# Performance work log

Hardware: AMD Instinct MI355X
Metric: run time of the kernel (lower is better)

## Reference

```python
import jax, jax.numpy as jnp
import numpy as np

N = 100000      # nodes
E = 1600000     # edges (avg degree 16)
IN = 128        # in_channels
OUT = 32        # out_channels -> hidden = 2*OUT = 64


def gcn_conv(x, src, dst, W, b):
    """PyG GCNConv: linear transform, add self loops, symmetric D^-1/2 (A+I) D^-1/2 aggregation."""
    n = x.shape[0]
    h = x @ W                                   # [N, out]
    # degree with self loops (all edge weights = 1)
    deg = jax.ops.segment_sum(jnp.ones(src.shape[0], h.dtype), dst, num_segments=n) + 1.0
    dinv = jax.lax.rsqrt(deg)                   # [N]
    norm = dinv[src] * dinv[dst]                # [E]
    agg = jax.ops.segment_sum(h[src] * norm[:, None], dst, num_segments=n)
    agg = agg + h * (dinv * dinv)[:, None]      # self-loop contribution
    return agg + b


def setup_inputs() -> dict:
    key = jax.random.key(0)
    ks = jax.random.split(key, 8)
    x = jax.random.normal(ks[0], (N, IN), jnp.float32)
    edge_index = jax.random.randint(ks[1], (2, E), 0, N, jnp.int32)
    H = 2 * OUT
    W1 = jax.random.normal(ks[2], (IN, H), jnp.float32) / jnp.sqrt(jnp.float32(IN))
    b1 = jnp.zeros((H,), jnp.float32)
    W_mu = jax.random.normal(ks[3], (H, OUT), jnp.float32) / jnp.sqrt(jnp.float32(H))
    b_mu = jnp.zeros((OUT,), jnp.float32)
    W_logstd = jax.random.normal(ks[4], (H, OUT), jnp.float32) / jnp.sqrt(jnp.float32(H))
    b_logstd = jnp.zeros((OUT,), jnp.float32)
    return {"x": x, "edge_index": edge_index, "W1": W1, "b1": b1,
            "W_mu": W_mu, "b_mu": b_mu, "W_logstd": W_logstd, "b_logstd": b_logstd}


def reference(x, edge_index, W1, b1, W_mu, b_mu, W_logstd, b_logstd):
    src, dst = edge_index[0], edge_index[1]
    h = jax.nn.relu(gcn_conv(x, src, dst, W1, b1))          # [N, 2*OUT]
    mu = gcn_conv(h, src, dst, W_mu, b_mu)                  # [N, OUT]
    logstd = gcn_conv(h, src, dst, W_logstd, b_logstd)      # [N, OUT]
    return mu, logstd
```

## Files before the change

### kernel.cpp

```cpp
#include <hip/hip_runtime.h>
#include <hip/hip_fp16.h>

#define IN_C 128
#define H 64
#define NBITS 9
#define BSZ 512
#define CAP 16384
#define BINCHUNK 4096
#define KC 32

typedef unsigned int u32;

__device__ __forceinline__ int excl_scan256(int v, int* wsum, int tid) {
    int lane = tid & 63, wid = tid >> 6;
    int s = v;
    #pragma unroll
    for (int off = 1; off < 64; off <<= 1) {
        int t = __shfl_up(s, off);
        if (lane >= off) s += t;
    }
    if (lane == 63) wsum[wid] = s;
    __syncthreads();
    if (tid == 0) {
        int c = 0;
        #pragma unroll
        for (int i = 0; i < 4; ++i) { int t = wsum[i]; wsum[i] = c; c += t; }
    }
    __syncthreads();
    return s - v + wsum[wid];
}

__device__ __forceinline__ int excl_scan512(int v, int* wsum, int tid) {
    int lane = tid & 63, wid = tid >> 6;
    int s = v;
    #pragma unroll
    for (int off = 1; off < 64; off <<= 1) {
        int t = __shfl_up(s, off);
        if (lane >= off) s += t;
    }
    if (lane == 63) wsum[wid] = s;
    __syncthreads();
    if (tid == 0) {
        int c = 0;
        #pragma unroll
        for (int i = 0; i < 8; ++i) { int t = wsum[i]; wsum[i] = c; c += t; }
    }
    __syncthreads();
    return s - v + wsum[wid];
}

__global__ __launch_bounds__(256) void k_init(int* __restrict__ bucketFill,
                                              __half* __restrict__ z0,
                                              __half* __restrict__ z1) {
    int tid = threadIdx.x;
    bucketFill[tid] = 0;
    if (tid < H) { z0[tid] = __float2half(0.f); z1[tid] = __float2half(0.f); }
}

__device__ __forceinline__ void mm1_tile(int tile, int t256, int n,
                                         const float* __restrict__ x,
                                         const float* __restrict__ W1,
                                         __half* __restrict__ out,
                                         float* __restrict__ sW,
                                         float* __restrict__ sxT) {
    const float4* W4 = (const float4*)W1;
    const float4* x4 = (const float4*)x;
    int base = tile * 64;
    int lane = t256 & 63, wave = t256 >> 6;
    int c0 = (lane & 15) << 2;
    int r0 = (wave << 4) | ((lane >> 4) << 2);
    float acc[4][4] = {};
    for (int kc = 0; kc < IN_C; kc += KC) {
        __syncthreads();
        for (int t = t256; t < KC * 16; t += 256)
            ((float4*)sW)[t] = W4[(kc + (t >> 4)) * 16 + (t & 15)];
        for (int t = t256; t < 512; t += 256) {
            int node = t >> 3, kq = t & 7;
            int gn = base + node;
            float4 vv = make_float4(0.f, 0.f, 0.f, 0.f);
            if (gn < n) vv = x4[(size_t)gn * 32 + (kc >> 2) + kq];
            int kl = kq << 2;
            sxT[(kl + 0) * 66 + node] = vv.x;
            sxT[(kl + 1) * 66 + node] = vv.y;
            sxT[(kl + 2) * 66 + node] = vv.z;
            sxT[(kl + 3) * 66 + node] = vv.w;
        }
        __syncthreads();
        #pragma unroll 8
        for (int k = 0; k < KC; ++k) {
            float2 xa = *(const float2*)&sxT[k * 66 + r0];
            float2 xb = *(const float2*)&sxT[k * 66 + r0 + 2];
            float4 wv = *(const float4*)&sW[k * 64 + c0];
            acc[0][0] += xa.x * wv.x; acc[0][1] += xa.x * wv.y; acc[0][2] += xa.x * wv.z; acc[0][3] += xa.x * wv.w;
            acc[1][0] += xa.y * wv.x; acc[1][1] += xa.y * wv.y; acc[1][2] += xa.y * wv.z; acc[1][3] += xa.y * wv.w;
            acc[2][0] += xb.x * wv.x; acc[2][1] += xb.x * wv.y; acc[2][2] += xb.x * wv.z; acc[2][3] += xb.x * wv.w;
            acc[3][0] += xb.y * wv.x; acc[3][1] += xb.y * wv.y; acc[3][2] += xb.y * wv.z; acc[3][3] += xb.y * wv.w;
        }
    }
    #pragma unroll
    for (int i = 0; i < 4; ++i) {
        int node = base + r0 + i;
        if (node < n) {
            union { uint2 u; __half2 h[2]; } pk;
            pk.h[0] = __floats2half2_rn(acc[i][0], acc[i][1]);
            pk.h[1] = __floats2half2_rn(acc[i][2], acc[i][3]);
            *(uint2*)&out[(size_t)node * 64 + c0] = pk.u;
        }
    }
}

union SMemBM {
    struct { u32 staged[BINCHUNK]; unsigned char stagedB[BINCHUNK];
             int lhist[256], lbase[256], gbase[256], lfill[256]; int wsum[4]; } bin;
    struct { float sW[KC * 64]; float sxT[KC * 66]; } mm;
};

__global__ __launch_bounds__(256) void k_binmm(const int* __restrict__ src,
                                               const int* __restrict__ dst,
                                               int E, int n, int nbin,
                                               int* __restrict__ bucketFill,
                                               u32* __restrict__ binned,
                                               const float* __restrict__ x,
                                               const float* __restrict__ W1,
                                               __half* __restrict__ Ah) {
    __shared__ SMemBM sm;
    int bid = blockIdx.x, tid = threadIdx.x;
    if (bid < nbin) {
        int kbeg = bid * BINCHUNK;
        int cnt = min(BINCHUNK, E - kbeg);
        sm.bin.lhist[tid] = 0; sm.bin.lfill[tid] = 0;
        __syncthreads();
        for (int t = tid; t < cnt; t += 256)
            atomicAdd(&sm.bin.lhist[dst[kbeg + t] >> NBITS], 1);
        __syncthreads();
        int v = sm.bin.lhist[tid];
        int ex = excl_scan256(v, sm.bin.wsum, tid);
        sm.bin.lbase[tid] = ex;
        sm.bin.gbase[tid] = v ? atomicAdd(&bucketFill[tid], v) : 0;
        __syncthreads();
        for (int t = tid; t < cnt; t += 256) {
            int d = dst[kbeg + t];
            int s = src[kbeg + t];
            int bk = d >> NBITS;
            int p = sm.bin.lbase[bk] + atomicAdd(&sm.bin.lfill[bk], 1);
            sm.bin.staged[p] = ((u32)(d & (BSZ - 1)) << 23) | (u32)s;
            sm.bin.stagedB[p] = (unsigned char)bk;
        }
        __syncthreads();
        for (int t = tid; t < cnt; t += 256) {
            int bk = sm.bin.stagedB[t];
            binned[(size_t)bk * CAP + sm.bin.gbase[bk] + (t - sm.bin.lbase[bk])] = sm.bin.staged[t];
        }
    } else {
        mm1_tile(bid - nbin, tid, n, x, W1, Ah, sm.mm.sW, sm.mm.sxT);
    }
}

__global__ __launch_bounds__(512) void k_bucket(const u32* __restrict__ binned,
                                                const int* __restrict__ bucketFill,
                                                u32* __restrict__ rowdesc,
                                                float* __restrict__ dinvp,
                                                int* __restrict__ colidx, int n) {
    __shared__ int cnt[BSZ];
    __shared__ int loff[BSZ];
    __shared__ int wsum[8];
    int b = blockIdx.x, tid = threadIdx.x;
    int ebeg = b * CAP;
    int fill = bucketFill[b];
    cnt[tid] = 0;
    __syncthreads();
    for (int e = tid; e < fill; e += 512)
        atomicAdd(&cnt[binned[ebeg + e] >> 23], 1);
    __syncthreads();
    int c0 = cnt[tid];
    int ex = excl_scan512(c0, wsum, tid);
    loff[tid] = ex;
    int node0 = (b << NBITS) + tid;
    if (node0 < n) {
        rowdesc[node0] = ((u32)(ebeg + ex) << 10) | (u32)min(c0, 1023);
        dinvp[node0] = rsqrtf((float)c0 + 1.0f);
    }
    __syncthreads();
    cnt[tid] = 0;
    __syncthreads();
    for (int e = tid; e < fill; e += 512) {
        u32 pv = binned[ebeg + e];
        int ln = pv >> 23;
        int pos = ebeg + loff[ln] + atomicAdd(&cnt[ln], 1);
        colidx[pos] = (int)(pv & 0x7FFFFF);
    }
}

template <bool L1, typename OutT>
__global__ __launch_bounds__(256) void k_gather(const __half* __restrict__ hs,
                                                OutT* __restrict__ out,
                                                const u32* __restrict__ rowdesc,
                                                const int* __restrict__ colidx,
                                                const float* __restrict__ dinv,
                                                const float* __restrict__ bias, int n) {
    int node = blockIdx.x * 4 + (threadIdx.x >> 6);
    if (node >= n) return;
    int lane = threadIdx.x & 63;
    int es = lane >> 4;
    int cc = lane & 15;
    u32 rd = rowdesc[node];
    int beg = (int)(rd >> 10);
    int deg = (int)(rd & 1023);
    int end = beg + deg;
    const uint2* hs4 = (const uint2*)hs;
    union U { uint2 u; __half2 h[2]; };

    int ci = n;
    float df = 0.f;
    if (lane < deg) {
        ci = colidx[beg + lane];
        if (L1) df = dinv[ci];
    }
    U selfr; selfr.u = hs4[(size_t)node * 16 + cc];
    float a0 = 0.f, a1 = 0.f, a2 = 0.f, a3 = 0.f;

    int m = min(deg, 64);
    {
        U r[4]; float d[4];
        #pragma unroll
        for (int j = 0; j < 4; ++j) {
            int idx = 4 * j + es;
            int s = __shfl(ci, idx);
            if (L1) d[j] = __shfl(df, idx);
            r[j].u = hs4[(size_t)s * 16 + cc];
        }
        #pragma unroll
        for (int j = 0; j < 4; ++j) {
            float2 f0 = __half22float2(r[j].h[0]);
            float2 f1 = __half22float2(r[j].h[1]);
            float w = L1 ? d[j] : 1.f;
            a0 += w * f0.x; a1 += w * f0.y; a2 += w * f1.x; a3 += w * f1.y;
        }
    }
    if (m > 16) {
        U r[4]; float d[4];
        #pragma unroll
        for (int j = 4; j < 8; ++j) {
            int idx = 4 * j + es;
            int s = __shfl(ci, idx);
            if (L1) d[j - 4] = __shfl(df, idx);
            r[j - 4].u = hs4[(size_t)s * 16 + cc];
        }
        #pragma unroll
        for (int j = 0; j < 4; ++j) {
            float2 f0 = __half22float2(r[j].h[0]);
            float2 f1 = __half22float2(r[j].h[1]);
            float w = L1 ? d[j] : 1.f;
            a0 += w * f0.x; a1 += w * f0.y; a2 += w * f1.x; a3 += w * f1.y;
        }
    }
    if (m > 32) {
        U r[8]; float d[8];
        #pragma unroll
        for (int j = 8; j < 16; ++j) {
            int idx = (4 * j + es) & 63;
            int s = __shfl(ci, idx);
            if (L1) d[j - 8] = __shfl(df, idx);
            r[j - 8].u = hs4[(size_t)s * 16 + cc];
        }
        #pragma unroll
        for (int j = 0; j < 8; ++j) {
            float2 f0 = __half22float2(r[j].h[0]);
            float2 f1 = __half22float2(r[j].h[1]);
            float w = L1 ? d[j] : 1.f;
            a0 += w * f0.x; a1 += w * f0.y; a2 += w * f1.x; a3 += w * f1.y;
        }
    }
    for (int e = beg + 64 + es; e < end; e += 4) {
        int s = colidx[e];
        U r; r.u = hs4[(size_t)s * 16 + cc];
        float w = L1 ? dinv[s] : 1.f;
        float2 f0 = __half22float2(r.h[0]);
        float2 f1 = __half22float2(r.h[1]);
        a0 += w * f0.x; a1 += w * f0.y; a2 += w * f1.x; a3 += w * f1.y;
    }
    a0 += __shfl_xor(a0, 16); a1 += __shfl_xor(a1, 16);
    a2 += __shfl_xor(a2, 16); a3 += __shfl_xor(a3, 16);
    a0 += __shfl_xor(a0, 32); a1 += __shfl_xor(a1, 32);
    a2 += __shfl_xor(a2, 32); a3 += __shfl_xor(a3, 32);

    if (lane < 16) {
        float di = dinv[node];
        float2 f0 = __half22float2(selfr.h[0]);
        float2 f1 = __half22float2(selfr.h[1]);
        float ws = L1 ? di : 1.f;
        a0 += ws * f0.x; a1 += ws * f0.y; a2 += ws * f1.x; a3 += ws * f1.y;
        float v0 = di * a0, v1 = di * a1, v2 = di * a2, v3 = di * a3;
        if (L1) {
            float4 bv = ((const float4*)bias)[cc];
            v0 = fmaxf(v0 + bv.x, 0.f) * di;
            v1 = fmaxf(v1 + bv.y, 0.f) * di;
            v2 = fmaxf(v2 + bv.z, 0.f) * di;
            v3 = fmaxf(v3 + bv.w, 0.f) * di;
        }
        if constexpr (sizeof(OutT) == 2) {
            U o;
            o.h[0] = __floats2half2_rn(v0, v1);
            o.h[1] = __floats2half2_rn(v2, v3);
            ((uint2*)out)[(size_t)node * 16 + cc] = o.u;
        } else {
            ((float4*)out)[(size_t)node * 16 + cc] = make_float4(v0, v1, v2, v3);
        }
    }
}

__global__ __launch_bounds__(256) void k_mm2(const float* __restrict__ g,
                                             const float* __restrict__ Wmu,
                                             const float* __restrict__ Wls,
                                             const float* __restrict__ bmu,
                                             const float* __restrict__ bls,
                                             float* __restrict__ out, int n) {
    __shared__ float sW[KC * 64];
    __shared__ float sgT[KC * 66];
    __shared__ float sb[64];
    int tid = threadIdx.x;
    int base = blockIdx.x * 64;
    if (tid < 64) sb[tid] = (tid < 32) ? bmu[tid] : bls[tid - 32];
    int lane = tid & 63, wave = tid >> 6;
    int c0 = (lane & 15) << 2;
    int r0 = (wave << 4) | ((lane >> 4) << 2);
    float acc[4][4] = {};

    for (int kc = 0; kc < H; kc += KC) {
        __syncthreads();
        for (int t = tid; t < KC * 16; t += 256) {
            int k = kc + (t >> 4), c = (t & 15) << 2;
            const float* srcp = (c < 32) ? (Wmu + k * 32 + c) : (Wls + k * 32 + (c - 32));
            ((float4*)sW)[t] = *(const float4*)srcp;
        }
        for (int t = tid; t < 512; t += 256) {
            int node = t >> 3, kq = t & 7;
            int gn = base + node;
            float4 vv = make_float4(0.f, 0.f, 0.f, 0.f);
            if (gn < n) vv = ((const float4*)g)[(size_t)gn * 16 + (kc >> 2) + kq];
            int kl = kq << 2;
            sgT[(kl + 0) * 66 + node] = vv.x;
            sgT[(kl + 1) * 66 + node] = vv.y;
            sgT[(kl + 2) * 66 + node] = vv.z;
            sgT[(kl + 3) * 66 + node] = vv.w;
        }
        __syncthreads();
        #pragma unroll 8
        for (int k = 0; k < KC; ++k) {
            float2 xa = *(const float2*)&sgT[k * 66 + r0];
            float2 xb = *(const float2*)&sgT[k * 66 + r0 + 2];
            float4 wv = *(const float4*)&sW[k * 64 + c0];
            acc[0][0] += xa.x * wv.x; acc[0][1] += xa.x * wv.y; acc[0][2] += xa.x * wv.z; acc[0][3] += xa.x * wv.w;
            acc[1][0] += xa.y * wv.x; acc[1][1] += xa.y * wv.y; acc[1][2] += xa.y * wv.z; acc[1][3] += xa.y * wv.w;
            acc[2][0] += xb.x * wv.x; acc[2][1] += xb.x * wv.y; acc[2][2] += xb.x * wv.z; acc[2][3] += xb.x * wv.w;
            acc[3][0] += xb.y * wv.x; acc[3][1] += xb.y * wv.y; acc[3][2] += xb.y * wv.z; acc[3][3] += xb.y * wv.w;
        }
    }
    #pragma unroll
    for (int i = 0; i < 4; ++i) {
        int node = base + r0 + i;
        if (node < n) {
            float4 o = make_float4(acc[i][0] + sb[c0], acc[i][1] + sb[c0 + 1],
                                   acc[i][2] + sb[c0 + 2], acc[i][3] + sb[c0 + 3]);
            if (c0 < 32) *(float4*)&out[(size_t)node * 32 + c0] = o;
            else *(float4*)&out[(size_t)n * 32 + (size_t)node * 32 + (c0 - 32)] = o;
        }
    }
}


extern "C" void kernel_launch(void* const* d_in, const int* in_sizes, int n_in,
                              void* d_out, int out_size, void* d_ws, size_t ws_size,
                              hipStream_t stream) {
    const float* x   = (const float*)d_in[0];
    const int*   ei  = (const int*)d_in[1];
    const float* W1  = (const float*)d_in[2];
    const float* b1  = (const float*)d_in[3];
    const float* Wmu = (const float*)d_in[4];
    const float* bmu = (const float*)d_in[5];
    const float* Wls = (const float*)d_in[6];
    const float* bls = (const float*)d_in[7];
    float* out = (float*)d_out;

    int n = in_sizes[0] / IN_C;
    int E = in_sizes[1] / 2;
    const int* srcp = ei;
    const int* dstp = ei + E;
    int NBUK = (n + BSZ - 1) >> NBITS;
    int nbin = (E + BINCHUNK - 1) / BINCHUNK;
    int ntiles = (n + 63) / 64;

    char* p = (char*)d_ws;
    __half* Ah  = (__half*)p; p += (size_t)(n + 1) * H * sizeof(__half);
    __half* Bh  = (__half*)p; p += (size_t)(n + 1) * H * sizeof(__half);
    float* G    = (float*)p;  p += (size_t)n * H * sizeof(float);
    float* dinv = (float*)p;  p += (size_t)n * sizeof(float);
    u32* rowdesc = (u32*)p;   p += (size_t)n * sizeof(u32);
    int* colidx = (int*)p;    p += (size_t)NBUK * CAP * sizeof(int);
    u32* binned = (u32*)p;    p += (size_t)NBUK * CAP * sizeof(u32);
    int* bucketFill = (int*)p; p += 256 * sizeof(int);

    k_init<<<1, 256, 0, stream>>>(bucketFill, Ah + (size_t)n * H, Bh + (size_t)n * H);
    k_binmm<<<nbin + ntiles, 256, 0, stream>>>(srcp, dstp, E, n, nbin,
                                               bucketFill, binned, x, W1, Ah);
    k_bucket<<<NBUK, 512, 0, stream>>>(binned, bucketFill, rowdesc, dinv, colidx, n);

    k_gather<true, __half><<<(n + 3) / 4, 256, 0, stream>>>(Ah, Bh, rowdesc, colidx, dinv, b1, n);
    k_gather<false, float><<<(n + 3) / 4, 256, 0, stream>>>(Bh, G, rowdesc, colidx, dinv, nullptr, n);
    k_mm2<<<(n + 63) / 64, 256, 0, stream>>>(G, Wmu, Wls, bmu, bls, out, n);
}
```

Baseline: 265.0 us.

## Use fp16 MFMA for both dense matmuls and store aggregated G in half

Replaces the scalar FP32 shared-memory GEMM tiles for the first layer transform and the mu/logstd projection with __builtin_amdgcn_mfma_f32_16x16x32_f16 matrix instructions. The weights are pre-transposed into fp16 in the init kernel, which now runs 16 blocks. The second aggregation now writes its output G in half precision, which halves that intermediate's traffic and lets mm2 load fp16 rows directly. The trade-off is extra fp16 rounding of x and G, plus scalar strided output stores in place of vectorized ones.

```diff
diff --git a/kernel.cpp b/kernel.cpp
--- a/kernel.cpp
+++ b/kernel.cpp
@@ -7,9 +7,10 @@
 #define BSZ 512
 #define CAP 16384
 #define BINCHUNK 4096
-#define KC 32
 
 typedef unsigned int u32;
+typedef __attribute__((ext_vector_type(8))) _Float16 h8;
+typedef __attribute__((ext_vector_type(4))) float f4;
 
 __device__ __forceinline__ int excl_scan256(int v, int* wsum, int tid) {
     int lane = tid & 63, wid = tid >> 6;
@@ -51,68 +52,69 @@
 
 __global__ __launch_bounds__(256) void k_init(int* __restrict__ bucketFill,
                                               __half* __restrict__ z0,
-                                              __half* __restrict__ z1) {
+                                              __half* __restrict__ z1,
+                                              const float* __restrict__ W1,
+                                              const float* __restrict__ Wmu,
+                                              const float* __restrict__ Wls,
+                                              _Float16* __restrict__ W1T,
+                                              _Float16* __restrict__ WT2) {
     int tid = threadIdx.x;
-    bucketFill[tid] = 0;
-    if (tid < H) { z0[tid] = __float2half(0.f); z1[tid] = __float2half(0.f); }
-}
-
-__device__ __forceinline__ void mm1_tile(int tile, int t256, int n,
-                                         const float* __restrict__ x,
-                                         const float* __restrict__ W1,
-                                         __half* __restrict__ out,
-                                         float* __restrict__ sW,
-                                         float* __restrict__ sxT) {
-    const float4* W4 = (const float4*)W1;
+    int gt = blockIdx.x * 256 + tid;
+    if (blockIdx.x == 0) {
+        bucketFill[tid] = 0;
+        if (tid < H) { z0[tid] = __float2half(0.f); z1[tid] = __float2half(0.f); }
+    }
+    for (int t = gt; t < 64 * 128; t += gridDim.x * 256) {
+        int col = t >> 7, k = t & 127;
+        W1T[t] = (_Float16)W1[k * 64 + col];
+    }
+    for (int t = gt; t < 64 * 64; t += gridDim.x * 256) {
+        int col = t >> 6, k = t & 63;
+        WT2[t] = (_Float16)((col < 32) ? Wmu[k * 32 + col] : Wls[k * 32 + (col - 32)]);
+    }
+}
+
+__device__ __forceinline__ void mm1_tile_mfma(int tile, int t256, int n,
+                                              const float* __restrict__ x,
+                                              const _Float16* __restrict__ W1T,
+                                              __half* __restrict__ out) {
+    int wave = t256 >> 6, lane = t256 & 63;
+    int cl = lane & 15;
+    int kg = lane >> 4;
+    int arow = tile * 64 + wave * 16 + cl;
+    int na = min(arow, n - 1);
     const float4* x4 = (const float4*)x;
-    int base = tile * 64;
-    int lane = t256 & 63, wave = t256 >> 6;
-    int c0 = (lane & 15) << 2;
-    int r0 = (wave << 4) | ((lane >> 4) << 2);
-    float acc[4][4] = {};
-    for (int kc = 0; kc < IN_C; kc += KC) {
-        __syncthreads();
-        for (int t = t256; t < KC * 16; t += 256)
-            ((float4*)sW)[t] = W4[(kc + (t >> 4)) * 16 + (t & 15)];
-        for (int t = t256; t < 512; t += 256) {
-            int node = t >> 3, kq = t & 7;
-            int gn = base + node;
-            float4 vv = make_float4(0.f, 0.f, 0.f, 0.f);
-            if (gn < n) vv = x4[(size_t)gn * 32 + (kc >> 2) + kq];
-            int kl = kq << 2;
-            sxT[(kl + 0) * 66 + node] = vv.x;
-            sxT[(kl + 1) * 66 + node] = vv.y;
-            sxT[(kl + 2) * 66 + node] = vv.z;
-            sxT[(kl + 3) * 66 + node] = vv.w;
-        }
-        __syncthreads();
-        #pragma unroll 8
-        for (int k = 0; k < KC; ++k) {
-            float2 xa = *(const float2*)&sxT[k * 66 + r0];
-            float2 xb = *(const float2*)&sxT[k * 66 + r0 + 2];
-            float4 wv = *(const float4*)&sW[k * 64 + c0];
-            acc[0][0] += xa.x * wv.x; acc[0][1] += xa.x * wv.y; acc[0][2] += xa.x * wv.z; acc[0][3] += xa.x * wv.w;
-            acc[1][0] += xa.y * wv.x; acc[1][1] += xa.y * wv.y; acc[1][2] += xa.y * wv.z; acc[1][3] += xa.y * wv.w;
-            acc[2][0] += xb.x * wv.x; acc[2][1] += xb.x * wv.y; acc[2][2] += xb.x * wv.z; acc[2][3] += xb.x * wv.w;
-            acc[3][0] += xb.y * wv.x; acc[3][1] += xb.y * wv.y; acc[3][2] += xb.y * wv.z; acc[3][3] += xb.y * wv.w;
-        }
-    }
-    #pragma unroll
-    for (int i = 0; i < 4; ++i) {
-        int node = base + r0 + i;
-        if (node < n) {
-            union { uint2 u; __half2 h[2]; } pk;
-            pk.h[0] = __floats2half2_rn(acc[i][0], acc[i][1]);
-            pk.h[1] = __floats2half2_rn(acc[i][2], acc[i][3]);
-            *(uint2*)&out[(size_t)node * 64 + c0] = pk.u;
-        }
-    }
-}
-
-union SMemBM {
-    struct { u32 staged[BINCHUNK]; unsigned char stagedB[BINCHUNK];
-             int lhist[256], lbase[256], gbase[256], lfill[256]; int wsum[4]; } bin;
-    struct { float sW[KC * 64]; float sxT[KC * 66]; } mm;
+    f4 zero4 = {0.f, 0.f, 0.f, 0.f};
+    f4 acc[4] = {zero4, zero4, zero4, zero4};
+    #pragma unroll
+    for (int kb = 0; kb < 4; ++kb) {
+        int k0 = kb * 32 + kg * 8;
+        float4 va = x4[(size_t)na * 32 + (k0 >> 2)];
+        float4 vb = x4[(size_t)na * 32 + (k0 >> 2) + 1];
+        h8 a;
+        a[0] = (_Float16)va.x; a[1] = (_Float16)va.y; a[2] = (_Float16)va.z; a[3] = (_Float16)va.w;
+        a[4] = (_Float16)vb.x; a[5] = (_Float16)vb.y; a[6] = (_Float16)vb.z; a[7] = (_Float16)vb.w;
+        #pragma unroll
+        for (int c = 0; c < 4; ++c) {
+            h8 b = *(const h8*)&W1T[((c * 16 + cl) << 7) + k0];
+            acc[c] = __builtin_amdgcn_mfma_f32_16x16x32_f16(a, b, acc[c], 0, 0, 0);
+        }
+    }
+    int rbase = tile * 64 + wave * 16 + kg * 4;
+    #pragma unroll
+    for (int r = 0; r < 4; ++r) {
+        int orow = rbase + r;
+        if (orow < n) {
+            #pragma unroll
+            for (int c = 0; c < 4; ++c)
+                out[(size_t)orow * 64 + c * 16 + cl] = __float2half((float)acc[c][r]);
+        }
+    }
+}
+
+struct SMemBin {
+    u32 staged[BINCHUNK]; unsigned char stagedB[BINCHUNK];
+    int lhist[256], lbase[256], gbase[256], lfill[256]; int wsum[4];
 };
 
 __global__ __launch_bounds__(256) void k_binmm(const int* __restrict__ src,
@@ -121,38 +123,38 @@
                                                int* __restrict__ bucketFill,
                                                u32* __restrict__ binned,
                                                const float* __restrict__ x,
-                                               const float* __restrict__ W1,
+                                               const _Float16* __restrict__ W1T,
                                                __half* __restrict__ Ah) {
-    __shared__ SMemBM sm;
+    __shared__ SMemBin sm;
     int bid = blockIdx.x, tid = threadIdx.x;
     if (bid < nbin) {
         int kbeg = bid * BINCHUNK;
         int cnt = min(BINCHUNK, E - kbeg);
-        sm.bin.lhist[tid] = 0; sm.bin.lfill[tid] = 0;
+        sm.lhist[tid] = 0; sm.lfill[tid] = 0;
         __syncthreads();
         for (int t = tid; t < cnt; t += 256)
-            atomicAdd(&sm.bin.lhist[dst[kbeg + t] >> NBITS], 1);
+            atomicAdd(&sm.lhist[dst[kbeg + t] >> NBITS], 1);
         __syncthreads();
-        int v = sm.bin.lhist[tid];
-        int ex = excl_scan256(v, sm.bin.wsum, tid);
-        sm.bin.lbase[tid] = ex;
-        sm.bin.gbase[tid] = v ? atomicAdd(&bucketFill[tid], v) : 0;
+        int v = sm.lhist[tid];
+        int ex = excl_scan256(v, sm.wsum, tid);
+        sm.lbase[tid] = ex;
+        sm.gbase[tid] = v ? atomicAdd(&bucketFill[tid], v) : 0;
         __syncthreads();
         for (int t = tid; t < cnt; t += 256) {
             int d = dst[kbeg + t];
             int s = src[kbeg + t];
             int bk = d >> NBITS;
-            int p = sm.bin.lbase[bk] + atomicAdd(&sm.bin.lfill[bk], 1);
-            sm.bin.staged[p] = ((u32)(d & (BSZ - 1)) << 23) | (u32)s;
-            sm.bin.stagedB[p] = (unsigned char)bk;
+            int p = sm.lbase[bk] + atomicAdd(&sm.lfill[bk], 1);
+            sm.staged[p] = ((u32)(d & (BSZ - 1)) << 23) | (u32)s;
+            sm.stagedB[p] = (unsigned char)bk;
         }
         __syncthreads();
         for (int t = tid; t < cnt; t += 256) {
-            int bk = sm.bin.stagedB[t];
-            binned[(size_t)bk * CAP + sm.bin.gbase[bk] + (t - sm.bin.lbase[bk])] = sm.bin.staged[t];
+            int bk = sm.stagedB[t];
+            binned[(size_t)bk * CAP + sm.gbase[bk] + (t - sm.lbase[bk])] = sm.staged[t];
         }
     } else {
-        mm1_tile(bid - nbin, tid, n, x, W1, Ah, sm.mm.sW, sm.mm.sxT);
+        mm1_tile_mfma(bid - nbin, tid, n, x, W1T, Ah);
     }
 }
 
@@ -309,61 +311,39 @@
     }
 }
 
-__global__ __launch_bounds__(256) void k_mm2(const float* __restrict__ g,
-                                             const float* __restrict__ Wmu,
-                                             const float* __restrict__ Wls,
+__global__ __launch_bounds__(256) void k_mm2(const __half* __restrict__ G,
+                                             const _Float16* __restrict__ WT2,
                                              const float* __restrict__ bmu,
                                              const float* __restrict__ bls,
                                              float* __restrict__ out, int n) {
-    __shared__ float sW[KC * 64];
-    __shared__ float sgT[KC * 66];
-    __shared__ float sb[64];
-    int tid = threadIdx.x;
-    int base = blockIdx.x * 64;
-    if (tid < 64) sb[tid] = (tid < 32) ? bmu[tid] : bls[tid - 32];
-    int lane = tid & 63, wave = tid >> 6;
-    int c0 = (lane & 15) << 2;
-    int r0 = (wave << 4) | ((lane >> 4) << 2);
-    float acc[4][4] = {};
-
-    for (int kc = 0; kc < H; kc += KC) {
-        __syncthreads();
-        for (int t = tid; t < KC * 16; t += 256) {
-            int k = kc + (t >> 4), c = (t & 15) << 2;
-            const float* srcp = (c < 32) ? (Wmu + k * 32 + c) : (Wls + k * 32 + (c - 32));
-            ((float4*)sW)[t] = *(const float4*)srcp;
-        }
-        for (int t = tid; t < 512; t += 256) {
-            int node = t >> 3, kq = t & 7;
-            int gn = base + node;
-            float4 vv = make_float4(0.f, 0.f, 0.f, 0.f);
-            if (gn < n) vv = ((const float4*)g)[(size_t)gn * 16 + (kc >> 2) + kq];
-            int kl = kq << 2;
-            sgT[(kl + 0) * 66 + node] = vv.x;
-            sgT[(kl + 1) * 66 + node] = vv.y;
-            sgT[(kl + 2) * 66 + node] = vv.z;
-            sgT[(kl + 3) * 66 + node] = vv.w;
-        }
-        __syncthreads();
-        #pragma unroll 8
-        for (int k = 0; k < KC; ++k) {
-            float2 xa = *(const float2*)&sgT[k * 66 + r0];
-            float2 xb = *(const float2*)&sgT[k * 66 + r0 + 2];
-            float4 wv = *(const float4*)&sW[k * 64 + c0];
-            acc[0][0] += xa.x * wv.x; acc[0][1] += xa.x * wv.y; acc[0][2] += xa.x * wv.z; acc[0][3] += xa.x * wv.w;
-            acc[1][0] += xa.y * wv.x; acc[1][1] += xa.y * wv.y; acc[1][2] += xa.y * wv.z; acc[1][3] += xa.y * wv.w;
-            acc[2][0] += xb.x * wv.x; acc[2][1] += xb.x * wv.y; acc[2][2] += xb.x * wv.z; acc[2][3] += xb.x * wv.w;
-            acc[3][0] += xb.y * wv.x; acc[3][1] += xb.y * wv.y; acc[3][2] += xb.y * wv.z; acc[3][3] += xb.y * wv.w;
-        }
-    }
-    #pragma unroll
-    for (int i = 0; i < 4; ++i) {
-        int node = base + r0 + i;
-        if (node < n) {
-            float4 o = make_float4(acc[i][0] + sb[c0], acc[i][1] + sb[c0 + 1],
-                                   acc[i][2] + sb[c0 + 2], acc[i][3] + sb[c0 + 3]);
-            if (c0 < 32) *(float4*)&out[(size_t)node * 32 + c0] = o;
-            else *(float4*)&out[(size_t)n * 32 + (size_t)node * 32 + (c0 - 32)] = o;
+    int tile = blockIdx.x;
+    int wave = threadIdx.x >> 6, lane = threadIdx.x & 63;
+    int cl = lane & 15, kg = lane >> 4;
+    int arow = tile * 64 + wave * 16 + cl;
+    int na = min(arow, n - 1);
+    const _Float16* Gf = (const _Float16*)G;
+    f4 zero4 = {0.f, 0.f, 0.f, 0.f};
+    f4 acc[4] = {zero4, zero4, zero4, zero4};
+    #pragma unroll
+    for (int kb = 0; kb < 2; ++kb) {
+        int k0 = kb * 32 + kg * 8;
+        h8 a = *(const h8*)&Gf[((size_t)na << 6) + k0];
+        #pragma unroll
+        for (int c = 0; c < 4; ++c) {
+            h8 b = *(const h8*)&WT2[((c * 16 + cl) << 6) + k0];
+            acc[c] = __builtin_amdgcn_mfma_f32_16x16x32_f16(a, b, acc[c], 0, 0, 0);
+        }
+    }
+    int rbase = tile * 64 + wave * 16 + kg * 4;
+    #pragma unroll
+    for (int c = 0; c < 4; ++c) {
+        int col = c * 16 + cl;
+        float bv = (col < 32) ? bmu[col] : bls[col - 32];
+        float* obase = (col < 32) ? (out + col) : (out + (size_t)n * 32 + (col - 32));
+        #pragma unroll
+        for (int r = 0; r < 4; ++r) {
+            int orow = rbase + r;
+            if (orow < n) obase[(size_t)orow * 32] = (float)acc[c][r] + bv;
         }
     }
 }
@@ -393,19 +373,22 @@
     char* p = (char*)d_ws;
     __half* Ah  = (__half*)p; p += (size_t)(n + 1) * H * sizeof(__half);
     __half* Bh  = (__half*)p; p += (size_t)(n + 1) * H * sizeof(__half);
-    float* G    = (float*)p;  p += (size_t)n * H * sizeof(float);
+    __half* G   = (__half*)p; p += (size_t)n * H * sizeof(__half);
     float* dinv = (float*)p;  p += (size_t)n * sizeof(float);
     u32* rowdesc = (u32*)p;   p += (size_t)n * sizeof(u32);
     int* colidx = (int*)p;    p += (size_t)NBUK * CAP * sizeof(int);
     u32* binned = (u32*)p;    p += (size_t)NBUK * CAP * sizeof(u32);
     int* bucketFill = (int*)p; p += 256 * sizeof(int);
-
-    k_init<<<1, 256, 0, stream>>>(bucketFill, Ah + (size_t)n * H, Bh + (size_t)n * H);
+    _Float16* W1T = (_Float16*)p; p += 64 * 128 * sizeof(_Float16);
+    _Float16* WT2 = (_Float16*)p; p += 64 * 64 * sizeof(_Float16);
+
+    k_init<<<16, 256, 0, stream>>>(bucketFill, Ah + (size_t)n * H, Bh + (size_t)n * H,
+                                   W1, Wmu, Wls, W1T, WT2);
     k_binmm<<<nbin + ntiles, 256, 0, stream>>>(srcp, dstp, E, n, nbin,
-                                               bucketFill, binned, x, W1, Ah);
+                                               bucketFill, binned, x, W1T, Ah);
     k_bucket<<<NBUK, 512, 0, stream>>>(binned, bucketFill, rowdesc, dinv, colidx, n);
 
     k_gather<true, __half><<<(n + 3) / 4, 256, 0, stream>>>(Ah, Bh, rowdesc, colidx, dinv, b1, n);
-    k_gather<false, float><<<(n + 3) / 4, 256, 0, stream>>>(Bh, G, rowdesc, colidx, dinv, nullptr, n);
-    k_mm2<<<(n + 63) / 64, 256, 0, stream>>>(G, Wmu, Wls, bmu, bls, out, n);
-}
+    k_gather<false, __half><<<(n + 3) / 4, 256, 0, stream>>>(Bh, G, rowdesc, colidx, dinv, nullptr, n);
+    k_mm2<<<(n + 63) / 64, 256, 0, stream>>>(G, WT2, bmu, bls, out, n);
+}
```

Measured after the change: 240.6 us. 1.1x faster.
